# Kernel tuning notes

Hardware: AMD Instinct MI355X
Metric: run time of the kernel (lower is better)

Reference implementation:

```python
import jax, jax.numpy as jnp
import numpy as np


def positional_encoding(n_tokens, d_model, dtype=jnp.float32):
    # standard sinusoidal PE: pe[pos, 2i] = sin(pos / 10000^(2i/d)), pe[pos, 2i+1] = cos(...)
    pos = jnp.arange(n_tokens, dtype=dtype)[:, None]            # [n, 1]
    i = jnp.arange(0, d_model, 2, dtype=dtype)[None, :]         # [1, d/2]
    angle = pos / jnp.power(jnp.asarray(10000.0, dtype), i / d_model)
    pe = jnp.zeros((n_tokens, d_model), dtype)
    pe = pe.at[:, 0::2].set(jnp.sin(angle))
    pe = pe.at[:, 1::2].set(jnp.cos(angle))
    return pe


def layer_norm(x, gamma, beta, eps=1e-5):
    mu = jnp.mean(x, axis=-1, keepdims=True)
    var = jnp.var(x, axis=-1, keepdims=True)
    return (x - mu) * jax.lax.rsqrt(var + eps) * gamma + beta


def setup_inputs() -> dict:
    key = jax.random.key(0)
    ks = jax.random.split(key, 4)
    b, n, d = 4, 1024, 1024
    dh = 1024  # dim_hidden_linear
    s = 1.0 / np.sqrt(d)
    return {
        "token_embedding": jax.random.normal(ks[0], (b, n, d), jnp.float32),
        "ln_gamma": jnp.ones((d,), jnp.float32),
        "ln_beta": jnp.zeros((d,), jnp.float32),
        "Wq": jax.random.normal(ks[1], (d, dh), jnp.float32) * s,
        "bq": jnp.zeros((dh,), jnp.float32),
        "Wk": jax.random.normal(ks[2], (d, dh), jnp.float32) * s,
        "bk": jnp.zeros((dh,), jnp.float32),
        "Wv": jax.random.normal(ks[3], (d, dh), jnp.float32) * s,
        "bv": jnp.zeros((dh,), jnp.float32),
        "num_heads": 16,
    }


def reference(token_embedding, ln_gamma, ln_beta, Wq, bq, Wk, bk, Wv, bv, num_heads):
    b, n, d = token_embedding.shape
    pe = positional_encoding(n, d)                      # [n, d]
    x = token_embedding + pe[None, :, :]                # broadcast over batch
    x = layer_norm(x, ln_gamma, ln_beta)
    q = x @ Wq + bq                                     # [b, n, dh]
    k = x @ Wk + bk
    v = x @ Wv + bv
    dh = q.shape[-1]
    hd = dh // num_heads                                # per-head dim
    q = q.reshape(b, n, num_heads, hd)
    k = k.reshape(b, n, num_heads, hd)
    v = v.reshape(b, n, num_heads, hd)
    scale = 1.0 / jnp.sqrt(jnp.asarray(hd, q.dtype))
    scores = jnp.einsum("bqhd,bkhd->bhqk", q, k) * scale  # [b, h, n, n]
    attn = jax.nn.softmax(scores, axis=-1)
    out = jnp.einsum("bhqk,bkhd->bqhd", attn, v)          # [b, n, h, hd]
    return out.reshape(b, n, dh)
```

## Files before the change

kernel.cpp:

```cpp
#include <hip/hip_runtime.h>
#include <hip/hip_bf16.h>
#include <math.h>

typedef __attribute__((ext_vector_type(8))) short bf16x8;
typedef __attribute__((ext_vector_type(4))) float f32x4;
typedef __attribute__((ext_vector_type(16))) float f32x16;

static __device__ __forceinline__ void gld16(const void* g, void* l) {
    __builtin_amdgcn_global_load_lds(
        (const __attribute__((address_space(1))) unsigned int*)g,
        (__attribute__((address_space(3))) unsigned int*)l, 16, 0, 0);
}

static __device__ __forceinline__ unsigned cvtpk(float lo, float hi) {
    unsigned r;
    asm("v_cvt_pk_bf16_f32 %0, %1, %2" : "=v"(r) : "v"(lo), "v"(hi));
    return r;
}

__global__ __launch_bounds__(256) void peln_wt_kernel(
    const float* __restrict__ emb,
    const float* __restrict__ gamma,
    const float* __restrict__ beta,
    const float* __restrict__ Wq,
    const float* __restrict__ Wk,
    const float* __restrict__ Wv,
    __hip_bfloat16* __restrict__ x,
    __hip_bfloat16* __restrict__ Wt)
{
    const int tid = threadIdx.x;
    if (blockIdx.x < 4096) {
        const int row = blockIdx.x;
        const int t   = row & 1023;
        float4 e = ((const float4*)(emb + (size_t)row * 1024))[tid];
        float v[4] = {e.x, e.y, e.z, e.w};
        float s = 0.f, ss = 0.f;
        #pragma unroll
        for (int kk = 0; kk < 4; ++kk) {
            int c = tid * 4 + kk;
            float ang = (float)t * exp2f(-13.287712379549449f * (float)(c >> 1) * (1.0f / 512.0f));
            float pe  = (c & 1) ? __cosf(ang) : __sinf(ang);
            v[kk] += pe;
            s  += v[kk];
            ss += v[kk] * v[kk];
        }
        #pragma unroll
        for (int off = 1; off < 64; off <<= 1) {
            s  += __shfl_xor(s, off);
            ss += __shfl_xor(ss, off);
        }
        __shared__ float red_s[4], red_ss[4];
        int wave = tid >> 6, lane = tid & 63;
        if (lane == 0) { red_s[wave] = s; red_ss[wave] = ss; }
        __syncthreads();
        float S  = red_s[0] + red_s[1] + red_s[2] + red_s[3];
        float SS = red_ss[0] + red_ss[1] + red_ss[2] + red_ss[3];
        float mu   = S * (1.0f / 1024.0f);
        float var  = SS * (1.0f / 1024.0f) - mu * mu;
        float rstd = rsqrtf(var + 1e-5f);
        #pragma unroll
        for (int kk = 0; kk < 4; ++kk) {
            int c = tid * 4 + kk;
            float y = (v[kk] - mu) * rstd * gamma[c] + beta[c];
            x[(size_t)row * 1024 + c] = __float2bfloat16(y);
        }
    } else {
        __shared__ __hip_bfloat16 tile[32][33];
        int wid = blockIdx.x - 4096;
        int zz  = wid >> 10;
        int rem = wid & 1023;
        int bx = rem & 31, by = rem >> 5;
        int tx = tid & 31, ty = tid >> 5;
        const float* src = (zz == 0) ? Wq : (zz == 1) ? Wk : Wv;
        __hip_bfloat16* dst = Wt + (size_t)zz * 1024 * 1024;
        int x0 = bx * 32, y0 = by * 32;
        #pragma unroll
        for (int kk = 0; kk < 4; ++kk)
            tile[ty + 8 * kk][tx] =
                __float2bfloat16(src[(size_t)(y0 + ty + 8 * kk) * 1024 + x0 + tx]);
        __syncthreads();
        #pragma unroll
        for (int kk = 0; kk < 4; ++kk)
            dst[(size_t)(x0 + ty + 8 * kk) * 1024 + y0 + tx] = tile[tx][ty + 8 * kk];
    }
}

__global__ __launch_bounds__(256) void qkv_gemm(
    const __hip_bfloat16* __restrict__ X,
    const __hip_bfloat16* __restrict__ Wt,
    const float* __restrict__ bq,
    const float* __restrict__ bk,
    const float* __restrict__ bv,
    __hip_bfloat16* __restrict__ qkv,
    __hip_bfloat16* __restrict__ vt)
{
    union SMem {
        struct { __hip_bfloat16 A[128 * 64]; __hip_bfloat16 B[128 * 64]; } s;
        __hip_bfloat16 C[128 * 132];
    };
    __shared__ __align__(16) SMem sm;

    const int id   = blockIdx.x;
    const int xcd  = id & 7;
    const int rest = id >> 3;
    const int j    = rest % 3;
    const int mblk = rest / 3;
    const int m0   = mblk * 128;
    const int n0   = (xcd * 3 + j) * 128;
    const int t    = n0 >> 10;
    const int nn0  = n0 & 1023;
    const __hip_bfloat16* W = Wt + (size_t)t * 1024 * 1024;

    const int tid  = threadIdx.x;
    const int wave = tid >> 6, lane = tid & 63;
    const int wm = wave & 1, wn = wave >> 1;
    const int lm = lane & 15, quad = lane >> 4;

    const int srow = lane >> 3;
    const int skc  = ((lane & 7) ^ srow) * 8;
    const int rbase = wave * 32;
    const __hip_bfloat16* gA = X + (size_t)(m0 + rbase + srow) * 1024 + skc;
    const __hip_bfloat16* gB = W + (size_t)(nn0 + rbase + srow) * 1024 + skc;
    __hip_bfloat16* lA = sm.s.A + rbase * 64;
    __hip_bfloat16* lB = sm.s.B + rbase * 64;

    f32x4 acc[4][4];
    #pragma unroll
    for (int i = 0; i < 4; ++i)
        #pragma unroll
        for (int jj = 0; jj < 4; ++jj)
            acc[i][jj] = (f32x4){0.f, 0.f, 0.f, 0.f};

    #pragma unroll
    for (int n = 0; n < 4; ++n) {
        gld16(gA + (size_t)n * 8 * 1024, lA + n * 8 * 64);
        gld16(gB + (size_t)n * 8 * 1024, lB + n * 8 * 64);
    }

    for (int k0 = 0; k0 < 1024; k0 += 64) {
        __syncthreads();

        bf16x8 a[2][4], b[2][4];
        #pragma unroll
        for (int ks = 0; ks < 2; ++ks) {
            #pragma unroll
            for (int i = 0; i < 4; ++i) {
                int row = wm * 64 + i * 16 + lm;
                a[ks][i] = *(const bf16x8*)(sm.s.A + (size_t)row * 64
                                            + (((ks * 4 + quad) ^ (lm & 7)) * 8));
            }
            #pragma unroll
            for (int jj = 0; jj < 4; ++jj) {
                int row = wn * 64 + jj * 16 + lm;
                b[ks][jj] = *(const bf16x8*)(sm.s.B + (size_t)row * 64
                                             + (((ks * 4 + quad) ^ (lm & 7)) * 8));
            }
        }
        __syncthreads();

        if (k0 + 64 < 1024) {
            #pragma unroll
            for (int n = 0; n < 4; ++n) {
                gld16(gA + (size_t)n * 8 * 1024 + k0 + 64, lA + n * 8 * 64);
                gld16(gB + (size_t)n * 8 * 1024 + k0 + 64, lB + n * 8 * 64);
            }
        }

        #pragma unroll
        for (int ks = 0; ks < 2; ++ks)
            #pragma unroll
            for (int i = 0; i < 4; ++i)
                #pragma unroll
                for (int jj = 0; jj < 4; ++jj)
                    acc[i][jj] = __builtin_amdgcn_mfma_f32_16x16x32_bf16(a[ks][i], b[ks][jj], acc[i][jj], 0, 0, 0);
    }

    const float* bias = (t == 0) ? bq : (t == 1) ? bk : bv;
    if (t < 2) {
        #pragma unroll
        for (int jj = 0; jj < 4; ++jj) {
            int col = wn * 64 + jj * 16 + lm;
            float bb = bias[nn0 + col];
            #pragma unroll
            for (int i = 0; i < 4; ++i)
                #pragma unroll
                for (int r = 0; r < 4; ++r) {
                    int row = wm * 64 + i * 16 + quad * 4 + r;
                    sm.C[(size_t)row * 132 + col] = __float2bfloat16(acc[i][jj][r] + bb);
                }
        }
        __syncthreads();
        __hip_bfloat16* out = qkv + (size_t)t * 4096 * 1024;
        #pragma unroll
        for (int c = 0; c < 8; ++c) {
            int g = tid + 256 * c;
            int row = g >> 4;
            int colc = (g & 15) * 8;
            bf16x8 vch = *(const bf16x8*)&sm.C[(size_t)row * 132 + colc];
            *(bf16x8*)(out + (size_t)(m0 + row) * 1024 + nn0 + colc) = vch;
        }
    } else {
        #pragma unroll
        for (int jj = 0; jj < 4; ++jj) {
            int col = wn * 64 + jj * 16 + lm;
            float bb = bias[nn0 + col];
            #pragma unroll
            for (int i = 0; i < 4; ++i)
                #pragma unroll
                for (int r = 0; r < 4; ++r) {
                    int row = wm * 64 + i * 16 + quad * 4 + r;
                    sm.C[(size_t)col * 132 + row] = __float2bfloat16(acc[i][jj][r] + bb);
                }
        }
        __syncthreads();
        const int bbase = (m0 >> 10) * 16 + (nn0 >> 6);
        const int mloc  = m0 & 1023;
        #pragma unroll
        for (int c = 0; c < 8; ++c) {
            int g = tid + 256 * c;
            int col = g >> 4;
            int rch = (g & 15) * 8;
            bf16x8 vch = *(const bf16x8*)&sm.C[(size_t)col * 132 + rch];
            int bh = bbase + (col >> 6);
            int d  = col & 63;
            *(bf16x8*)(vt + ((size_t)bh * 64 + d) * 1024 + mloc + rch) = vch;
        }
    }
}

__global__ __launch_bounds__(256, 2) void attn_kernel(
    const __hip_bfloat16* __restrict__ q,
    const __hip_bfloat16* __restrict__ k,
    const __hip_bfloat16* __restrict__ vt,
    float* __restrict__ out)
{
    __shared__ __align__(16) __hip_bfloat16 Kbuf[2][128 * 64];
    __shared__ __align__(16) __hip_bfloat16 Vbuf[2][2][64 * 64];
    const int id   = blockIdx.x;
    const int bh   = (id & 7) * 8 + ((id >> 3) & 7);
    const int qblk = id >> 6;
    const int b = bh >> 4, h = bh & 15;
    const int wave = threadIdx.x >> 6, lane = threadIdx.x & 63;
    const int l31 = lane & 31, hi5 = lane >> 5;
    const int qbase = qblk * 128 + wave * 32;
    const float CEXP = 0.18033688011112042f;

    bf16x8 bq32[4];
    #pragma unroll
    for (int slab = 0; slab < 4; ++slab)
        bq32[slab] = *(const bf16x8*)(q + (size_t)(b * 1024 + qbase + l31) * 1024
                                        + h * 64 + (slab * 2 + hi5) * 8);

    const __hip_bfloat16* kg = k + (size_t)(b * 1024) * 1024 + h * 64;
    const __hip_bfloat16* vg = vt + (size_t)bh * 64 * 1024;
    const int srow = lane >> 3;
    const int skc  = ((lane & 7) ^ srow) * 8;

    f32x16 OT[2];
    #pragma unroll
    for (int dt = 0; dt < 2; ++dt)
        #pragma unroll
        for (int r = 0; r < 16; ++r)
            OT[dt][r] = 0.f;
    float li = 0.f;

    auto stageKV = [&](int buf, int kt) {
        #pragma unroll
        for (int n = 0; n < 4; ++n) {
            int r0 = wave * 32 + n * 8;
            gld16(kg + (size_t)(kt + r0 + srow) * 1024 + skc, Kbuf[buf] + r0 * 64);
        }
        int half = wave >> 1;
        #pragma unroll
        for (int n = 0; n < 4; ++n) {
            int d0 = (wave & 1) * 32 + n * 8;
            gld16(vg + (size_t)(d0 + srow) * 1024 + kt + half * 64 + skc,
                  Vbuf[buf][half] + d0 * 64);
        }
    };

    stageKV(0, 0);

    for (int tt = 0; tt < 8; ++tt) {
        __syncthreads();
        if (tt + 1 < 8) stageKV((tt + 1) & 1, (tt + 1) * 128);

        const __hip_bfloat16* Kb = Kbuf[tt & 1];

        #pragma unroll
        for (int sr = 0; sr < 2; ++sr) {
            const __hip_bfloat16* Vb = Vbuf[tt & 1][sr];

            f32x16 ST[2];
            #pragma unroll
            for (int kt = 0; kt < 2; ++kt) {
                #pragma unroll
                for (int r = 0; r < 16; ++r) ST[kt][r] = 0.f;
                #pragma unroll
                for (int slab = 0; slab < 4; ++slab) {
                    bf16x8 ak = *(const bf16x8*)(Kb
                        + (size_t)(sr * 64 + kt * 32 + l31) * 64
                        + (((slab * 2 + hi5) ^ (l31 & 7)) * 8));
                    ST[kt] = __builtin_amdgcn_mfma_f32_32x32x16_bf16(ak, bq32[slab], ST[kt], 0, 0, 0);
                }
            }

            unsigned pw[4][4];
            #pragma unroll
            for (int kt = 0; kt < 2; ++kt) {
                float pv[16];
                #pragma unroll
                for (int r = 0; r < 16; ++r) {
                    pv[r] = __builtin_amdgcn_exp2f(ST[kt][r] * CEXP);
                    li += pv[r];
                }
                #pragma unroll
                for (int s = 0; s < 2; ++s) {
                    unsigned P0 = cvtpk(pv[8 * s + 0], pv[8 * s + 1]);
                    unsigned P1 = cvtpk(pv[8 * s + 2], pv[8 * s + 3]);
                    unsigned P2 = cvtpk(pv[8 * s + 4], pv[8 * s + 5]);
                    unsigned P3 = cvtpk(pv[8 * s + 6], pv[8 * s + 7]);
                    asm("v_permlane32_swap_b32 %0, %1" : "+v"(P0), "+v"(P2));
                    asm("v_permlane32_swap_b32 %0, %1" : "+v"(P1), "+v"(P3));
                    int ks = kt * 2 + s;
                    pw[ks][0] = P0; pw[ks][1] = P1; pw[ks][2] = P2; pw[ks][3] = P3;
                }
            }

            #pragma unroll
            for (int dt = 0; dt < 2; ++dt)
                #pragma unroll
                for (int ks = 0; ks < 4; ++ks) {
                    bf16x8 av = *(const bf16x8*)(Vb
                        + (size_t)(dt * 32 + l31) * 64
                        + (((ks * 2 + hi5) ^ (l31 & 7)) * 8));
                    bf16x8 pf;
                    __builtin_memcpy(&pf, pw[ks], 16);
                    OT[dt] = __builtin_amdgcn_mfma_f32_32x32x16_bf16(av, pf, OT[dt], 0, 0, 0);
                }
        }
    }

    li += __shfl_xor(li, 32);
    float inv = 1.0f / li;
    const int qrow = qbase + l31;

    #pragma unroll
    for (int dt = 0; dt < 2; ++dt)
        #pragma unroll
        for (int g = 0; g < 4; ++g) {
            float4 o4 = {OT[dt][4 * g + 0] * inv, OT[dt][4 * g + 1] * inv,
                         OT[dt][4 * g + 2] * inv, OT[dt][4 * g + 3] * inv};
            *(float4*)(out + (size_t)(b * 1024 + qrow) * 1024
                       + h * 64 + dt * 32 + 8 * g + 4 * hi5) = o4;
        }
}

extern "C" void kernel_launch(void* const* d_in, const int* in_sizes, int n_in,
                              void* d_out, int out_size, void* d_ws, size_t ws_size,
                              hipStream_t stream)
{
    const float* emb   = (const float*)d_in[0];
    const float* gamma = (const float*)d_in[1];
    const float* beta  = (const float*)d_in[2];
    const float* Wq    = (const float*)d_in[3];
    const float* bq    = (const float*)d_in[4];
    const float* Wk    = (const float*)d_in[5];
    const float* bk    = (const float*)d_in[6];
    const float* Wv    = (const float*)d_in[7];
    const float* bv    = (const float*)d_in[8];
    float* out = (float*)d_out;

    __hip_bfloat16* ws  = (__hip_bfloat16*)d_ws;
    __hip_bfloat16* x   = ws;
    __hip_bfloat16* Wt  = x   + (size_t)4096 * 1024;
    __hip_bfloat16* qkv = Wt  + (size_t)3 * 1024 * 1024;
    __hip_bfloat16* vt  = qkv + (size_t)2 * 4096 * 1024;

    peln_wt_kernel<<<4096 + 3072, 256, 0, stream>>>(emb, gamma, beta, Wq, Wk, Wv, x, Wt);
    qkv_gemm<<<768, 256, 0, stream>>>(x, Wt, bq, bk, bv, qkv, vt);
    attn_kernel<<<512, 256, 0, stream>>>(qkv, qkv + (size_t)4096 * 1024, vt, out);
}
```

Measured before the change: 149.7 us.

## Load K and V tiles directly from global memory instead of LDS staging

Removes the double-buffered LDS staging of K and V tiles (global_load_lds plus __syncthreads) from the attention kernel. Each wave now reads its K and V MFMA operands straight from global memory (relying on L1/L2 caching) in 64-key chunks. This drops the shared-memory footprint and the barriers, which may allow more occupancy. In exchange, the four waves in a block each fetch the same K/V data redundantly, and the loads are strided 16-byte accesses without explicit prefetch, so latency is exposed.

```diff
diff --git a/kernel.cpp b/kernel.cpp
--- a/kernel.cpp
+++ b/kernel.cpp
@@ -234,8 +234,6 @@
     const __hip_bfloat16* __restrict__ vt,
     float* __restrict__ out)
 {
-    __shared__ __align__(16) __hip_bfloat16 Kbuf[2][128 * 64];
-    __shared__ __align__(16) __hip_bfloat16 Vbuf[2][2][64 * 64];
     const int id   = blockIdx.x;
     const int bh   = (id & 7) * 8 + ((id >> 3) & 7);
     const int qblk = id >> 6;
@@ -253,8 +251,6 @@
 
     const __hip_bfloat16* kg = k + (size_t)(b * 1024) * 1024 + h * 64;
     const __hip_bfloat16* vg = vt + (size_t)bh * 64 * 1024;
-    const int srow = lane >> 3;
-    const int skc  = ((lane & 7) ^ srow) * 8;
 
     f32x16 OT[2];
     #pragma unroll
@@ -264,81 +260,54 @@
             OT[dt][r] = 0.f;
     float li = 0.f;
 
-    auto stageKV = [&](int buf, int kt) {
-        #pragma unroll
-        for (int n = 0; n < 4; ++n) {
-            int r0 = wave * 32 + n * 8;
-            gld16(kg + (size_t)(kt + r0 + srow) * 1024 + skc, Kbuf[buf] + r0 * 64);
-        }
-        int half = wave >> 1;
-        #pragma unroll
-        for (int n = 0; n < 4; ++n) {
-            int d0 = (wave & 1) * 32 + n * 8;
-            gld16(vg + (size_t)(d0 + srow) * 1024 + kt + half * 64 + skc,
-                  Vbuf[buf][half] + d0 * 64);
-        }
-    };
-
-    stageKV(0, 0);
-
-    for (int tt = 0; tt < 8; ++tt) {
-        __syncthreads();
-        if (tt + 1 < 8) stageKV((tt + 1) & 1, (tt + 1) * 128);
-
-        const __hip_bfloat16* Kb = Kbuf[tt & 1];
-
-        #pragma unroll
-        for (int sr = 0; sr < 2; ++sr) {
-            const __hip_bfloat16* Vb = Vbuf[tt & 1][sr];
-
-            f32x16 ST[2];
-            #pragma unroll
-            for (int kt = 0; kt < 2; ++kt) {
-                #pragma unroll
-                for (int r = 0; r < 16; ++r) ST[kt][r] = 0.f;
-                #pragma unroll
-                for (int slab = 0; slab < 4; ++slab) {
-                    bf16x8 ak = *(const bf16x8*)(Kb
-                        + (size_t)(sr * 64 + kt * 32 + l31) * 64
-                        + (((slab * 2 + hi5) ^ (l31 & 7)) * 8));
-                    ST[kt] = __builtin_amdgcn_mfma_f32_32x32x16_bf16(ak, bq32[slab], ST[kt], 0, 0, 0);
-                }
-            }
-
-            unsigned pw[4][4];
-            #pragma unroll
-            for (int kt = 0; kt < 2; ++kt) {
-                float pv[16];
-                #pragma unroll
-                for (int r = 0; r < 16; ++r) {
-                    pv[r] = __builtin_amdgcn_exp2f(ST[kt][r] * CEXP);
-                    li += pv[r];
-                }
-                #pragma unroll
-                for (int s = 0; s < 2; ++s) {
-                    unsigned P0 = cvtpk(pv[8 * s + 0], pv[8 * s + 1]);
-                    unsigned P1 = cvtpk(pv[8 * s + 2], pv[8 * s + 3]);
-                    unsigned P2 = cvtpk(pv[8 * s + 4], pv[8 * s + 5]);
-                    unsigned P3 = cvtpk(pv[8 * s + 6], pv[8 * s + 7]);
-                    asm("v_permlane32_swap_b32 %0, %1" : "+v"(P0), "+v"(P2));
-                    asm("v_permlane32_swap_b32 %0, %1" : "+v"(P1), "+v"(P3));
-                    int ks = kt * 2 + s;
-                    pw[ks][0] = P0; pw[ks][1] = P1; pw[ks][2] = P2; pw[ks][3] = P3;
-                }
-            }
-
-            #pragma unroll
-            for (int dt = 0; dt < 2; ++dt)
-                #pragma unroll
-                for (int ks = 0; ks < 4; ++ks) {
-                    bf16x8 av = *(const bf16x8*)(Vb
-                        + (size_t)(dt * 32 + l31) * 64
-                        + (((ks * 2 + hi5) ^ (l31 & 7)) * 8));
-                    bf16x8 pf;
-                    __builtin_memcpy(&pf, pw[ks], 16);
-                    OT[dt] = __builtin_amdgcn_mfma_f32_32x32x16_bf16(av, pf, OT[dt], 0, 0, 0);
-                }
-        }
+    for (int kc = 0; kc < 1024; kc += 64) {
+        f32x16 ST[2];
+        #pragma unroll
+        for (int kt = 0; kt < 2; ++kt) {
+            #pragma unroll
+            for (int r = 0; r < 16; ++r) ST[kt][r] = 0.f;
+            #pragma unroll
+            for (int slab = 0; slab < 4; ++slab) {
+                bf16x8 ak = *(const bf16x8*)(kg
+                    + (size_t)(kc + kt * 32 + l31) * 1024
+                    + (slab * 2 + hi5) * 8);
+                ST[kt] = __builtin_amdgcn_mfma_f32_32x32x16_bf16(ak, bq32[slab], ST[kt], 0, 0, 0);
+            }
+        }
+
+        unsigned pw[4][4];
+        #pragma unroll
+        for (int kt = 0; kt < 2; ++kt) {
+            float pv[16];
+            #pragma unroll
+            for (int r = 0; r < 16; ++r) {
+                pv[r] = __builtin_amdgcn_exp2f(ST[kt][r] * CEXP);
+                li += pv[r];
+            }
+            #pragma unroll
+            for (int s = 0; s < 2; ++s) {
+                unsigned P0 = cvtpk(pv[8 * s + 0], pv[8 * s + 1]);
+                unsigned P1 = cvtpk(pv[8 * s + 2], pv[8 * s + 3]);
+                unsigned P2 = cvtpk(pv[8 * s + 4], pv[8 * s + 5]);
+                unsigned P3 = cvtpk(pv[8 * s + 6], pv[8 * s + 7]);
+                asm("v_permlane32_swap_b32 %0, %1" : "+v"(P0), "+v"(P2));
+                asm("v_permlane32_swap_b32 %0, %1" : "+v"(P1), "+v"(P3));
+                int ks = kt * 2 + s;
+                pw[ks][0] = P0; pw[ks][1] = P1; pw[ks][2] = P2; pw[ks][3] = P3;
+            }
+        }
+
+        #pragma unroll
+        for (int dt = 0; dt < 2; ++dt)
+            #pragma unroll
+            for (int ks = 0; ks < 4; ++ks) {
+                bf16x8 av = *(const bf16x8*)(vg
+                    + (size_t)(dt * 32 + l31) * 1024
+                    + kc + (ks * 2 + hi5) * 8);
+                bf16x8 pf;
+                __builtin_memcpy(&pf, pw[ks], 16);
+                OT[dt] = __builtin_amdgcn_mfma_f32_32x32x16_bf16(av, pf, OT[dt], 0, 0, 0);
+            }
     }
 
     li += __shfl_xor(li, 32);
```

Measured after the change: 184.1 us. +23.0%, slower.
